# Performance work log

Hardware: AMD Instinct MI355X
Metric: run time of the kernel (lower is better)

Reference implementation:

```python
import jax, jax.numpy as jnp
import numpy as np

B, S, IN, E, H, FF, L = 8, 1024, 128, 512, 8, 2048, 4
HD = E // H
EPS = 1e-5


def make_pe(seq_len, d_model):
    position = np.arange(seq_len, dtype=np.float32)[:, None]
    div_term = np.exp(np.arange(0, d_model, 2, dtype=np.float32) * (-np.log(10000.0) / d_model))
    pe = np.zeros((seq_len, d_model), dtype=np.float32)
    pe[:, 0::2] = np.sin(position * div_term)
    pe[:, 1::2] = np.cos(position * div_term)
    return jnp.asarray(pe)


def setup_inputs() -> dict:
    key = jax.random.key(0)
    ks = jax.random.split(key, 16)
    s = 0.02
    return {
        "src": jax.random.normal(ks[0], (B, S, IN), jnp.float32),
        "distances": jax.random.uniform(ks[1], (B, S, S), jnp.float32),
        "proj_w": jax.random.normal(ks[2], (E, IN), jnp.float32) * s,
        "proj_b": jnp.zeros((E,), jnp.float32),
        "bn_g": jnp.ones((E,), jnp.float32),
        "bn_b": jnp.zeros((E,), jnp.float32),
        "in_proj_w": jax.random.normal(ks[3], (3 * E, E), jnp.float32) * s,
        "in_proj_b": jnp.zeros((3 * E,), jnp.float32),
        "dist_scale": jnp.array(1.0, jnp.float32),
        "lin1_w": jax.random.normal(ks[4], (FF, E), jnp.float32) * s,
        "lin1_b": jnp.zeros((FF,), jnp.float32),
        "lin2_w": jax.random.normal(ks[5], (E, FF), jnp.float32) * s,
        "lin2_b": jnp.zeros((E,), jnp.float32),
        "n1_g": jnp.ones((E,), jnp.float32),
        "n1_b": jnp.zeros((E,), jnp.float32),
        "n2_g": jnp.ones((E,), jnp.float32),
        "n2_b": jnp.zeros((E,), jnp.float32),
    }


def layernorm(x, g, b):
    m = jnp.mean(x, axis=-1, keepdims=True)
    v = jnp.var(x, axis=-1, keepdims=True)
    return (x - m) * jax.lax.rsqrt(v + EPS) * g + b


def reference(src, distances, proj_w, proj_b, bn_g, bn_b, in_proj_w, in_proj_b,
              dist_scale, lin1_w, lin1_b, lin2_w, lin2_b, n1_g, n1_b, n2_g, n2_b):
    # input projection
    x = jnp.einsum('bsi,ei->bse', src, proj_w) + proj_b  # [B,S,E]
    # BatchNorm1d over flattened (B*S) dim, training-mode batch stats
    xf = x.reshape(-1, E)
    mu = jnp.mean(xf, axis=0)
    var = jnp.var(xf, axis=0)
    x = ((xf - mu) * jax.lax.rsqrt(var + EPS) * bn_g + bn_b).reshape(B, S, E)
    # positional encoding
    x = x + make_pe(S, E)[None]
    # distance bias (same for every layer)
    dmax = jnp.max(distances, axis=-1, keepdims=True)
    dist_bias = jnp.exp(dist_scale * (1.0 - distances / dmax))  # [B,S,S]
    scale = 1.0 / jnp.sqrt(jnp.float32(HD))
    # num_layers iterations of the SAME (shared-parameter) layer
    for _ in range(L):
        qkv = jnp.einsum('bse,fe->bsf', x, in_proj_w) + in_proj_b  # [B,S,3E]
        q, k, v = jnp.split(qkv, 3, axis=-1)
        q = q.reshape(B, S, H, HD).transpose(0, 2, 1, 3)
        k = k.reshape(B, S, H, HD).transpose(0, 2, 1, 3)
        scores = jnp.einsum('bhqd,bhkd->bhqk', q, k) * scale  # [B,H,S,S]
        attn = jax.nn.softmax(scores, axis=-1)
        avg_w = jnp.mean(attn, axis=1)  # head-averaged weights [B,S,S]
        w = avg_w * dist_bias
        w = w / jnp.sum(w, axis=-1, keepdims=True)
        # NOTE: original bmm uses raw layer input as value (no V/out projection)
        attn_out = jnp.einsum('bqk,bke->bqe', w, x)
        x = layernorm(x + attn_out, n1_g, n1_b)
        ff = jnp.einsum('bsf,ef->bse', jax.nn.relu(jnp.einsum('bse,fe->bsf', x, lin1_w) + lin1_b), lin2_w) + lin2_b
        x = layernorm(x + ff, n2_g, n2_b)
    return x
```

## Files before the change

### kernel.cpp

```cpp
#include <hip/hip_runtime.h>
#include <hip/hip_bf16.h>
#include <math.h>

#define Bz 8
#define Sz 1024
#define INz 128
#define Ez 512
#define Hz 8
#define HDz 64
#define FFz 2048
#define Lz 4
#define Nz (Bz*Sz)
#define EPSf 1e-5f

typedef __attribute__((ext_vector_type(8))) short short8;
typedef __attribute__((ext_vector_type(4))) float floatx4;
#define MFMA16(a,b,c) __builtin_amdgcn_mfma_f32_16x16x32_bf16(a,b,c,0,0,0)

typedef __hip_bfloat16 bf16;

__device__ inline float b2f(bf16 v) { return __bfloat162float(v); }
__device__ inline bf16 f2b(float v) { return __float2bfloat16(v); }

__device__ inline void gload16(const bf16* g, bf16* lds_base)
{
  __builtin_amdgcn_global_load_lds(
      (const __attribute__((address_space(1))) void*)g,
      (__attribute__((address_space(3))) void*)lds_base,
      16, 0, 0);
}

#define FENCE() asm volatile("" ::: "memory")
#define PB() do { FENCE(); __builtin_amdgcn_s_barrier(); FENCE(); } while (0)
#define VMCNT0() asm volatile("s_waitcnt vmcnt(0)" ::: "memory")
#define VMCNT8() asm volatile("s_waitcnt vmcnt(8)" ::: "memory")

__global__ __launch_bounds__(256) void cast_f2b(const float* __restrict__ in,
    bf16* __restrict__ out, int n)
{
  int i = blockIdx.x * 256 + threadIdx.x;
  if (i < n) out[i] = f2b(in[i]);
}

__global__ __launch_bounds__(512, 1) void gemm256(
    const bf16* __restrict__ A, const bf16* __restrict__ Wm,
    const float* __restrict__ bias, bf16* __restrict__ Cb,
    int N, int K, int relu)
{
  int gx = gridDim.x, nwg = gx * gridDim.y;
  int flat = blockIdx.y * gx + blockIdx.x;
  if (!(nwg & 7)) {
    int cpx = nwg >> 3;
    flat = (flat & 7) * cpx + (flat >> 3);
  }
  int bm = (flat / gx) * 256, bn = (flat % gx) * 256;
  __shared__ __align__(16) bf16 As0[256][64], Bs0[256][64];
  __shared__ __align__(16) bf16 As1[256][64], Bs1[256][64];
  int t = threadIdx.x, wave = t >> 6, lane = t & 63;
  int wm = (wave >> 2) * 128, wn = (wave & 3) * 64;
  int fr = lane & 15, fo = lane >> 4;
  int w8 = wave * 8, lrow = lane >> 3;
  int sc8 = ((lane & 7) ^ (lrow & 7)) * 8;
  floatx4 acc[8][4];
  #pragma unroll
  for (int i = 0; i < 8; ++i)
    #pragma unroll
    for (int j = 0; j < 4; ++j) acc[i][j] = (floatx4){0.f, 0.f, 0.f, 0.f};

  #define STAGE8(DA, DB, kk) do {                                           \
    _Pragma("unroll")                                                        \
    for (int c_ = 0; c_ < 4; ++c_) {                                         \
      int row_ = c_ * 64 + w8 + lrow;                                        \
      gload16(A  + (size_t)(bm + row_) * K + (kk) + sc8, &DA[c_ * 64 + w8][0]);\
      gload16(Wm + (size_t)(bn + row_) * K + (kk) + sc8, &DB[c_ * 64 + w8][0]);\
    } } while (0)

  #define TILE(AA, BB, SA, SB, kk, DOSTAGE) do {                            \
    _Pragma("unroll")                                                        \
    for (int q_ = 0; q_ < 4; ++q_) {                                         \
      short8 a_[4][2], bf_[2][2];                                            \
      _Pragma("unroll")                                                      \
      for (int j_ = 0; j_ < 4; ++j_) {                                       \
        int row_ = wm + ((q_ >> 1) * 4 + j_) * 16 + fr;                      \
        a_[j_][0] = *(const short8*)&AA[row_][((fo) ^ (fr & 7)) * 8];        \
        a_[j_][1] = *(const short8*)&AA[row_][((4 + fo) ^ (fr & 7)) * 8];    \
      }                                                                      \
      _Pragma("unroll")                                                      \
      for (int g_ = 0; g_ < 2; ++g_) {                                       \
        int row_ = wn + ((q_ & 1) * 2 + g_) * 16 + fr;                       \
        bf_[g_][0] = *(const short8*)&BB[row_][((fo) ^ (fr & 7)) * 8];       \
        bf_[g_][1] = *(const short8*)&BB[row_][((4 + fo) ^ (fr & 7)) * 8];   \
      }                                                                      \
      if ((DOSTAGE) && q_ == 0) STAGE8(SA, SB, kk);                          \
      PB();                                                                  \
      __builtin_amdgcn_s_setprio(1);                                         \
      _Pragma("unroll")                                                      \
      for (int j_ = 0; j_ < 4; ++j_)                                         \
        _Pragma("unroll")                                                    \
        for (int g_ = 0; g_ < 2; ++g_) {                                     \
          int fi_ = (q_ >> 1) * 4 + j_, gi_ = (q_ & 1) * 2 + g_;             \
          acc[fi_][gi_] = MFMA16(a_[j_][0], bf_[g_][0], acc[fi_][gi_]);      \
          acc[fi_][gi_] = MFMA16(a_[j_][1], bf_[g_][1], acc[fi_][gi_]);      \
        }                                                                    \
      __builtin_amdgcn_s_setprio(0);                                         \
      if (q_ == 3) VMCNT0();                                                 \
      PB();                                                                  \
    } } while (0)

  int nt = K >> 6;
  STAGE8(As0, Bs0, 0);
  STAGE8(As1, Bs1, 64);
  VMCNT8();
  PB();
  TILE(As0, Bs0, As0, Bs0, 0, 0);
  for (int i = 1; i + 2 < nt; i += 2) {
    TILE(As1, Bs1, As0, Bs0, (i + 1) * 64, 1);
    TILE(As0, Bs0, As1, Bs1, (i + 2) * 64, 1);
  }
  TILE(As1, Bs1, As0, Bs0, 0, 0);
  #undef STAGE8
  #undef TILE

  #pragma unroll
  for (int f = 0; f < 8; ++f) {
    #pragma unroll
    for (int r = 0; r < 4; ++r) {
      int row = bm + wm + f * 16 + (lane >> 4) * 4 + r;
      #pragma unroll
      for (int g = 0; g < 4; ++g) {
        int col = bn + wn + g * 16 + fr;
        float v = acc[f][g][r] + (bias ? bias[col] : 0.f);
        if (relu) v = fmaxf(v, 0.f);
        Cb[(size_t)row * N + col] = f2b(v);
      }
    }
  }
}

__global__ __launch_bounds__(256) void gemm_bt(
    const bf16* __restrict__ A, const bf16* __restrict__ Wm,
    const float* __restrict__ bias, float* __restrict__ Cf,
    bf16* __restrict__ Cb, const float* __restrict__ rowscale,
    int M, int N, int K, long sA, long sW, long sC, int relu)
{
  int z = blockIdx.z;
  A  += (size_t)z * sA;
  Wm += (size_t)z * sW;
  if (rowscale) rowscale += (size_t)z * M;
  size_t cbase = (size_t)z * sC;
  int bm = blockIdx.y * 128, bn = blockIdx.x * 128;
  __shared__ __align__(16) bf16 As0[128][64], Bs0[128][64];
  __shared__ __align__(16) bf16 As1[128][64], Bs1[128][64];
  int t = threadIdx.x, wave = t >> 6, lane = t & 63;
  int wm = (wave >> 1) * 64, wn = (wave & 1) * 64;
  int fr = lane & 15, fo = lane >> 4;
  int srow = lane >> 3;
  int scol = ((lane & 7) ^ srow) * 8;
  floatx4 acc[4][4];
  #pragma unroll
  for (int i = 0; i < 4; ++i)
    #pragma unroll
    for (int j = 0; j < 4; ++j) acc[i][j] = (floatx4){0.f, 0.f, 0.f, 0.f};

  #define STAGE(Ad, Bd, kk) do {                                            \
    _Pragma("unroll")                                                        \
    for (int i_ = 0; i_ < 4; ++i_) {                                         \
      int chunk_ = wave * 4 + i_;                                            \
      int row_ = chunk_ * 8 + srow;                                          \
      gload16(A  + (size_t)(bm + row_) * K + (kk) + scol, &Ad[chunk_ * 8][0]);\
      gload16(Wm + (size_t)(bn + row_) * K + (kk) + scol, &Bd[chunk_ * 8][0]);\
    } } while (0)

  #define COMPUTE(Ad, Bd) do {                                               \
    _Pragma("unroll")                                                        \
    for (int ks_ = 0; ks_ < 2; ++ks_) {                                      \
      int sw_ = ((ks_ * 4 + fo) ^ (fr & 7)) * 8;                             \
      short8 af_[4], bf_[4];                                                 \
      _Pragma("unroll")                                                      \
      for (int rt_ = 0; rt_ < 4; ++rt_)                                      \
        af_[rt_] = *(const short8*)&Ad[wm + rt_ * 16 + fr][sw_];             \
      _Pragma("unroll")                                                      \
      for (int ct_ = 0; ct_ < 4; ++ct_)                                      \
        bf_[ct_] = *(const short8*)&Bd[wn + ct_ * 16 + fr][sw_];             \
      _Pragma("unroll")                                                      \
      for (int rt_ = 0; rt_ < 4; ++rt_)                                      \
        _Pragma("unroll")                                                    \
        for (int ct_ = 0; ct_ < 4; ++ct_)                                    \
          acc[rt_][ct_] = MFMA16(af_[rt_], bf_[ct_], acc[rt_][ct_]);         \
    } } while (0)

  STAGE(As0, Bs0, 0);
  __syncthreads();
  for (int k0 = 0; k0 < K; k0 += 128) {
    if (k0 + 64 < K) STAGE(As1, Bs1, k0 + 64);
    COMPUTE(As0, Bs0);
    __syncthreads();
    if (k0 + 64 < K) {
      if (k0 + 128 < K) STAGE(As0, Bs0, k0 + 128);
      COMPUTE(As1, Bs1);
      __syncthreads();
    }
  }
  #undef STAGE
  #undef COMPUTE

  #pragma unroll
  for (int rt = 0; rt < 4; ++rt) {
    #pragma unroll
    for (int r = 0; r < 4; ++r) {
      int row = bm + wm + rt * 16 + (lane >> 4) * 4 + r;
      float rs = rowscale ? (1.f / rowscale[row]) : 1.f;
      #pragma unroll
      for (int ct = 0; ct < 4; ++ct) {
        int col = bn + wn + ct * 16 + fr;
        float v = acc[rt][ct][r] + (bias ? bias[col] : 0.f);
        if (relu) v = fmaxf(v, 0.f);
        v *= rs;
        if (Cf) Cf[cbase + (size_t)row * N + col] = v;
        if (Cb) Cb[cbase + (size_t)row * N + col] = f2b(v);
      }
    }
  }
}

__global__ __launch_bounds__(256) void bn_stats(const float* __restrict__ x, float* __restrict__ st)
{
  int c = blockIdx.x;
  float s = 0.f, q = 0.f;
  for (int r = threadIdx.x; r < Nz; r += 256) {
    float v = x[(size_t)r * Ez + c];
    s += v; q += v * v;
  }
  for (int o = 32; o; o >>= 1) { s += __shfl_down(s, o); q += __shfl_down(q, o); }
  __shared__ float shs[4], shq[4];
  int w = threadIdx.x >> 6;
  if ((threadIdx.x & 63) == 0) { shs[w] = s; shq[w] = q; }
  __syncthreads();
  if (threadIdx.x == 0) {
    s = shs[0] + shs[1] + shs[2] + shs[3];
    q = shq[0] + shq[1] + shq[2] + shq[3];
    float mu = s / (float)Nz;
    float var = q / (float)Nz - mu * mu;
    st[c] = mu;
    st[Ez + c] = rsqrtf(var + EPSf);
  }
}

__global__ __launch_bounds__(256) void bn_apply_pe(const float* __restrict__ x0,
    const float* __restrict__ st, const float* __restrict__ g,
    const float* __restrict__ b, float* __restrict__ x, bf16* __restrict__ xb)
{
  int idx = blockIdx.x * 256 + threadIdx.x;
  int c = idx & (Ez - 1);
  int r = idx >> 9;
  int s = r & (Sz - 1);
  float dt = expf((float)(c & ~1) * (-9.210340371976184f / (float)Ez));
  float ang = (float)s * dt;
  float pe = (c & 1) ? cosf(ang) : sinf(ang);
  float mu = st[c], rs = st[Ez + c];
  float v = (x0[idx] - mu) * rs * g[c] + b[c] + pe;
  x[idx] = v;
  xb[idx] = f2b(v);
}

__global__ __launch_bounds__(256) void dist_bias_k(const float* __restrict__ dist,
    const float* __restrict__ dsc, bf16* __restrict__ db)
{
  size_t base = (size_t)blockIdx.x * Sz;
  float m = -1e30f;
  for (int j = threadIdx.x; j < Sz; j += 256) m = fmaxf(m, dist[base + j]);
  for (int o = 32; o; o >>= 1) m = fmaxf(m, __shfl_down(m, o));
  __shared__ float sh[4];
  if ((threadIdx.x & 63) == 0) sh[threadIdx.x >> 6] = m;
  __syncthreads();
  m = fmaxf(fmaxf(sh[0], sh[1]), fmaxf(sh[2], sh[3]));
  float sc = dsc[0];
  float inv = 1.f / m;
  for (int j = threadIdx.x; j < Sz; j += 256)
    db[base + j] = f2b(expf(sc * (1.f - dist[base + j] * inv)));
}

__global__ __launch_bounds__(256) void transpose_xb(const bf16* __restrict__ xb,
    bf16* __restrict__ xT)
{
  int b = blockIdx.z, e0 = blockIdx.y * 32, s0 = blockIdx.x * 32;
  __shared__ bf16 T[32][40];
  int t = threadIdx.x, row = t >> 3, c = t & 7;
  *(ushort4*)&T[row][c * 4] = *(const ushort4*)(xb + (size_t)(b * Sz + s0 + row) * Ez + e0 + c * 4);
  __syncthreads();
  ushort4 v;
  unsigned short* vp = (unsigned short*)&v;
  #pragma unroll
  for (int i = 0; i < 4; ++i) vp[i] = *(const unsigned short*)&T[c * 4 + i][row];
  *(ushort4*)(xT + ((size_t)b * Ez + e0 + row) * Sz + s0 + c * 4) = v;
}

__global__ __launch_bounds__(256) void attn_stats2(const bf16* __restrict__ qk,
    float* __restrict__ stats, float* __restrict__ den)
{
  int qt = blockIdx.x, h = blockIdx.y, b = blockIdx.z;
  int q0 = qt * 64;
  int t = threadIdx.x, wave = t >> 6, lane = t & 63;
  if (h == 0 && t < 64) den[(size_t)b * Sz + q0 + t] = 0.f;
  __shared__ bf16 Qs[64][72];
  __shared__ bf16 Ks[128][72];
  int fr = lane & 15, fo = (lane >> 4) * 8;
  #pragma unroll
  for (int i = 0; i < 2; ++i) {
    int idx = i * 256 + t, row = idx >> 3, c4 = idx & 7;
    *(float4*)&Qs[row][c4 * 8] =
      *(const float4*)(qk + (size_t)(b * Sz + q0 + row) * 1024 + h * 64 + c4 * 8);
  }
  __syncthreads();
  short8 aq0 = *(const short8*)&Qs[wave * 16 + fr][fo];
  short8 aq1 = *(const short8*)&Qs[wave * 16 + fr][32 + fo];
  float m_run[4] = {-1e30f, -1e30f, -1e30f, -1e30f};
  float z_run[4] = {0.f, 0.f, 0.f, 0.f};
  for (int k0 = 0; k0 < Sz; k0 += 128) {
    __syncthreads();
    #pragma unroll
    for (int i = 0; i < 4; ++i) {
      int idx = i * 256 + t, row = idx >> 3, c4 = idx & 7;
      *(float4*)&Ks[row][c4 * 8] =
        *(const float4*)(qk + (size_t)(b * Sz + k0 + row) * 1024 + 512 + h * 64 + c4 * 8);
    }
    __syncthreads();
    float sc[8][4];
    #pragma unroll
    for (int j = 0; j < 8; ++j) {
      floatx4 a4 = (floatx4){0.f, 0.f, 0.f, 0.f};
      short8 b0 = *(const short8*)&Ks[j * 16 + fr][fo];
      short8 b1 = *(const short8*)&Ks[j * 16 + fr][32 + fo];
      a4 = MFMA16(aq0, b0, a4);
      a4 = MFMA16(aq1, b1, a4);
      #pragma unroll
      for (int r = 0; r < 4; ++r) sc[j][r] = a4[r] * 0.125f;
    }
    #pragma unroll
    for (int r = 0; r < 4; ++r) {
      float vm = sc[0][r];
      #pragma unroll
      for (int j = 1; j < 8; ++j) vm = fmaxf(vm, sc[j][r]);
      #pragma unroll
      for (int o = 1; o < 16; o <<= 1) vm = fmaxf(vm, __shfl_xor(vm, o, 16));
      float mn = fmaxf(m_run[r], vm);
      float zb = 0.f;
      #pragma unroll
      for (int j = 0; j < 8; ++j) zb += __expf(sc[j][r] - mn);
      #pragma unroll
      for (int o = 1; o < 16; o <<= 1) zb += __shfl_xor(zb, o, 16);
      z_run[r] = z_run[r] * __expf(m_run[r] - mn) + zb;
      m_run[r] = mn;
    }
  }
  if (fr == 0) {
    int qb = q0 + wave * 16 + (lane >> 4) * 4;
    #pragma unroll
    for (int r = 0; r < 4; ++r) {
      size_t o = ((size_t)(b * Hz + h) * Sz + qb + r) * 2;
      stats[o] = m_run[r];
      stats[o + 1] = z_run[r];
    }
  }
}

__global__ __launch_bounds__(256) void scores_bias(const bf16* __restrict__ qk,
    const bf16* __restrict__ db, const float* __restrict__ stats,
    bf16* __restrict__ aw, float* __restrict__ den)
{
  int kt = blockIdx.x, qt = blockIdx.y, b = blockIdx.z;
  int q0 = qt * 128, k0 = kt * 128;
  __shared__ bf16 Qs[128][72];
  __shared__ bf16 Ks[128][72];
  __shared__ float mS[128][9];
  __shared__ float ziS[128][9];
  int t = threadIdx.x, wave = t >> 6, lane = t & 63;
  int fr = lane & 15, fo = (lane >> 4) * 8;
  int wm = (wave >> 1) * 64, wn = (wave & 1) * 64;

  #pragma unroll
  for (int i = 0; i < 4; ++i) {
    int lin = i * 256 + t, h = lin >> 7, q = lin & 127;
    const float* sp = stats + ((size_t)(b * Hz + h) * Sz + q0 + q) * 2;
    mS[q][h] = sp[0];
    ziS[q][h] = 1.f / sp[1];
  }

  floatx4 pac[4][4];
  #pragma unroll
  for (int i = 0; i < 4; ++i)
    #pragma unroll
    for (int j = 0; j < 4; ++j) pac[i][j] = (floatx4){0.f, 0.f, 0.f, 0.f};

  for (int h = 0; h < 8; ++h) {
    __syncthreads();
    #pragma unroll
    for (int i = 0; i < 4; ++i) {
      int idx = i * 256 + t, row = idx >> 3, c4 = idx & 7;
      *(float4*)&Qs[row][c4 * 8] =
        *(const float4*)(qk + (size_t)(b * Sz + q0 + row) * 1024 + h * 64 + c4 * 8);
      *(float4*)&Ks[row][c4 * 8] =
        *(const float4*)(qk + (size_t)(b * Sz + k0 + row) * 1024 + 512 + h * 64 + c4 * 8);
    }
    __syncthreads();
    short8 bfv0[4], bfv1[4];
    #pragma unroll
    for (int ct = 0; ct < 4; ++ct) {
      bfv0[ct] = *(const short8*)&Ks[wn + ct * 16 + fr][fo];
      bfv1[ct] = *(const short8*)&Ks[wn + ct * 16 + fr][32 + fo];
    }
    #pragma unroll
    for (int rt = 0; rt < 4; ++rt) {
      short8 af0 = *(const short8*)&Qs[wm + rt * 16 + fr][fo];
      short8 af1 = *(const short8*)&Qs[wm + rt * 16 + fr][32 + fo];
      floatx4 sc[4];
      #pragma unroll
      for (int ct = 0; ct < 4; ++ct) {
        floatx4 z4 = (floatx4){0.f, 0.f, 0.f, 0.f};
        z4 = MFMA16(af0, bfv0[ct], z4);
        sc[ct] = MFMA16(af1, bfv1[ct], z4);
      }
      #pragma unroll
      for (int r = 0; r < 4; ++r) {
        int qloc = wm + rt * 16 + (lane >> 4) * 4 + r;
        float m = mS[qloc][h], zi = ziS[qloc][h];
        #pragma unroll
        for (int ct = 0; ct < 4; ++ct)
          pac[rt][ct][r] += __expf(sc[ct][r] * 0.125f - m) * zi;
      }
    }
  }

  #pragma unroll
  for (int rt = 0; rt < 4; ++rt) {
    #pragma unroll
    for (int r = 0; r < 4; ++r) {
      int qloc = wm + rt * 16 + (lane >> 4) * 4 + r;
      size_t rowoff = (size_t)(b * Sz + q0 + qloc) * Sz + k0;
      float rsum = 0.f;
      #pragma unroll
      for (int ct = 0; ct < 4; ++ct) {
        int kloc = wn + ct * 16 + fr;
        float p = pac[rt][ct][r] * 0.125f * b2f(db[rowoff + kloc]);
        aw[rowoff + kloc] = f2b(p);
        rsum += p;
      }
      #pragma unroll
      for (int o = 1; o < 16; o <<= 1) rsum += __shfl_xor(rsum, o, 16);
      if (fr == 0) atomicAdd(den + (size_t)b * Sz + q0 + qloc, rsum);
    }
  }
}

__global__ __launch_bounds__(256) void add_ln(const float* __restrict__ xin,
    const float* __restrict__ dly, const float* __restrict__ g,
    const float* __restrict__ bb, float* __restrict__ xout, bf16* __restrict__ xbout)
{
  size_t base = (size_t)blockIdx.x * Ez;
  int t = threadIdx.x;
  float2 xi = *(const float2*)(xin + base + t * 2);
  float2 dl = *(const float2*)(dly + base + t * 2);
  float a0 = xi.x + dl.x;
  float a1 = xi.y + dl.y;
  float s = a0 + a1, q = a0 * a0 + a1 * a1;
  for (int o = 32; o; o >>= 1) { s += __shfl_down(s, o); q += __shfl_down(q, o); }
  __shared__ float shs[4], shq[4];
  if ((t & 63) == 0) { shs[t >> 6] = s; shq[t >> 6] = q; }
  __syncthreads();
  s = shs[0] + shs[1] + shs[2] + shs[3];
  q = shq[0] + shq[1] + shq[2] + shq[3];
  float mu = s * (1.f / Ez);
  float var = q * (1.f / Ez) - mu * mu;
  float rs = rsqrtf(var + EPSf);
  float v0 = (a0 - mu) * rs * g[t * 2] + bb[t * 2];
  float v1 = (a1 - mu) * rs * g[t * 2 + 1] + bb[t * 2 + 1];
  float2 vo; vo.x = v0; vo.y = v1;
  *(float2*)(xout + base + t * 2) = vo;
  bf16 b0 = f2b(v0), b1 = f2b(v1);
  ushort2 pk;
  pk.x = *(unsigned short*)&b0;
  pk.y = *(unsigned short*)&b1;
  *(ushort2*)(xbout + base + t * 2) = pk;
}

extern "C" void kernel_launch(void* const* d_in, const int* in_sizes, int n_in,
                              void* d_out, int out_size, void* d_ws, size_t ws_size,
                              hipStream_t stream)
{
  const float* src        = (const float*)d_in[0];
  const float* distances  = (const float*)d_in[1];
  const float* proj_w     = (const float*)d_in[2];
  const float* proj_b     = (const float*)d_in[3];
  const float* bn_g       = (const float*)d_in[4];
  const float* bn_b       = (const float*)d_in[5];
  const float* in_proj_w  = (const float*)d_in[6];
  const float* in_proj_b  = (const float*)d_in[7];
  const float* dist_scale = (const float*)d_in[8];
  const float* lin1_w     = (const float*)d_in[9];
  const float* lin1_b     = (const float*)d_in[10];
  const float* lin2_w     = (const float*)d_in[11];
  const float* lin2_b     = (const float*)d_in[12];
  const float* n1_g       = (const float*)d_in[13];
  const float* n1_b       = (const float*)d_in[14];
  const float* n2_g       = (const float*)d_in[15];
  const float* n2_b       = (const float*)d_in[16];

  float* x = (float*)d_out;

  float* stats = (float*)d_ws;
  float* den   = stats + 131072;
  float* bnst  = den + 8192;
  float* aout  = bnst + 1024;
  float* x0    = aout;
  bf16* db_b = (bf16*)(aout + (size_t)Nz * Ez);
  bf16* Rqk  = db_b + (size_t)Bz * Sz * Sz;
  bf16* qk   = Rqk;
  bf16* aw   = Rqk + (size_t)Nz * 1024;
  bf16* ff1  = Rqk;
  bf16* xb   = Rqk + (size_t)Nz * FFz;
  bf16* xT   = xb + (size_t)Nz * Ez;
  bf16* srcb = xT + (size_t)Bz * Ez * Sz;
  bf16* wpr  = srcb + (size_t)Nz * INz;
  bf16* wqk  = wpr + Ez * INz;
  bf16* wl1  = wqk + 1024 * Ez;
  bf16* wl2  = wl1 + FFz * Ez;

  cast_f2b<<<(Nz * INz) / 256, 256, 0, stream>>>(src, srcb, Nz * INz);
  cast_f2b<<<(Ez * INz + 255) / 256, 256, 0, stream>>>(proj_w, wpr, Ez * INz);
  cast_f2b<<<(1024 * Ez) / 256, 256, 0, stream>>>(in_proj_w, wqk, 1024 * Ez);
  cast_f2b<<<(FFz * Ez) / 256, 256, 0, stream>>>(lin1_w, wl1, FFz * Ez);
  cast_f2b<<<(Ez * FFz) / 256, 256, 0, stream>>>(lin2_w, wl2, Ez * FFz);

  gemm_bt<<<dim3(Ez / 128, Nz / 128, 1), 256, 0, stream>>>(
      srcb, wpr, proj_b, x0, nullptr, nullptr, Nz, Ez, INz, 0, 0, 0, 0);
  bn_stats<<<Ez, 256, 0, stream>>>(x0, bnst);
  bn_apply_pe<<<(Nz * Ez) / 256, 256, 0, stream>>>(x0, bnst, bn_g, bn_b, x, xb);
  dist_bias_k<<<Bz * Sz, 256, 0, stream>>>(distances, dist_scale, db_b);

  for (int l = 0; l < Lz; ++l) {
    transpose_xb<<<dim3(Sz / 32, Ez / 32, Bz), 256, 0, stream>>>(xb, xT);
    gemm_bt<<<dim3(1024 / 128, Nz / 128, 1), 256, 0, stream>>>(
        xb, wqk, in_proj_b, nullptr, qk, nullptr, Nz, 1024, Ez, 0, 0, 0, 0);
    attn_stats2<<<dim3(Sz / 64, Hz, Bz), 256, 0, stream>>>(qk, stats, den);
    scores_bias<<<dim3(Sz / 128, Sz / 128, Bz), 256, 0, stream>>>(qk, db_b, stats, aw, den);
    gemm_bt<<<dim3(Ez / 128, Sz / 128, Bz), 256, 0, stream>>>(
        aw, xT, nullptr, aout, nullptr, den,
        Sz, Ez, Sz, (long)Sz * Sz, (long)Ez * Sz, (long)Sz * Ez, 0);
    add_ln<<<Nz, 256, 0, stream>>>(x, aout, n1_g, n1_b, x, xb);
    gemm256<<<dim3(FFz / 256, Nz / 256), 512, 0, stream>>>(
        xb, wl1, lin1_b, ff1, FFz, Ez, 1);
    gemm_bt<<<dim3(Ez / 128, Nz / 128, 1), 256, 0, stream>>>(
        ff1, wl2, lin2_b, aout, nullptr, nullptr, Nz, Ez, FFz, 0, 0, 0, 0);
    add_ln<<<Nz, 256, 0, stream>>>(x, aout, n2_g, n2_b, x, xb);
  }
}
```

Measured before the change: 1.138 ms.

## Double-buffer Q/K tiles with async direct-to-LDS loads and XOR swizzle

Rewrites the attention stats and score-bias kernels to stage Q/K tiles with gload16 (global-to-LDS loads) into two LDS buffers. The load of the next tile overlaps the MFMA and softmax work on the current one. The padded [72] LDS rows become unpadded [64] rows with an XOR swizzle to avoid bank conflicts. In exchange it doubles LDS use per block, which may lower occupancy, and it relies on the swizzle matching between the stores and the fragment reads.

```diff
diff --git a/kernel.cpp b/kernel.cpp
--- a/kernel.cpp
+++ b/kernel.cpp
@@ -302,57 +302,73 @@
   int q0 = qt * 64;
   int t = threadIdx.x, wave = t >> 6, lane = t & 63;
   if (h == 0 && t < 64) den[(size_t)b * Sz + q0 + t] = 0.f;
-  __shared__ bf16 Qs[64][72];
-  __shared__ bf16 Ks[128][72];
-  int fr = lane & 15, fo = (lane >> 4) * 8;
+  __shared__ __align__(16) bf16 Qs[64][64];
+  __shared__ __align__(16) bf16 Ks0[128][64], Ks1[128][64];
+  int fr = lane & 15, fo = lane >> 4;
+  int srow = lane >> 3;
+  int scol = ((lane & 7) ^ srow) * 8;
+  int sw0 = ((fo) ^ (fr & 7)) * 8, sw1 = ((4 + fo) ^ (fr & 7)) * 8;
+
   #pragma unroll
   for (int i = 0; i < 2; ++i) {
-    int idx = i * 256 + t, row = idx >> 3, c4 = idx & 7;
-    *(float4*)&Qs[row][c4 * 8] =
-      *(const float4*)(qk + (size_t)(b * Sz + q0 + row) * 1024 + h * 64 + c4 * 8);
-  }
-  __syncthreads();
-  short8 aq0 = *(const short8*)&Qs[wave * 16 + fr][fo];
-  short8 aq1 = *(const short8*)&Qs[wave * 16 + fr][32 + fo];
+    int chunk = wave * 2 + i, row = chunk * 8 + srow;
+    gload16(qk + (size_t)(b * Sz + q0 + row) * 1024 + h * 64 + scol, &Qs[chunk * 8][0]);
+  }
+  #define STAGEK(Kd, kk) do {                                                \
+    _Pragma("unroll")                                                        \
+    for (int i_ = 0; i_ < 4; ++i_) {                                         \
+      int chunk_ = wave * 4 + i_, row_ = chunk_ * 8 + srow;                  \
+      gload16(qk + (size_t)(b * Sz + (kk) + row_) * 1024 + 512 + h * 64 + scol,\
+              &Kd[chunk_ * 8][0]);                                           \
+    } } while (0)
+
+  STAGEK(Ks0, 0);
+  __syncthreads();
+  short8 aq0 = *(const short8*)&Qs[wave * 16 + fr][sw0];
+  short8 aq1 = *(const short8*)&Qs[wave * 16 + fr][sw1];
   float m_run[4] = {-1e30f, -1e30f, -1e30f, -1e30f};
   float z_run[4] = {0.f, 0.f, 0.f, 0.f};
-  for (int k0 = 0; k0 < Sz; k0 += 128) {
+
+  #define KCOMP(Kd) do {                                                     \
+    float sc[8][4];                                                          \
+    _Pragma("unroll")                                                        \
+    for (int j = 0; j < 8; ++j) {                                            \
+      floatx4 a4 = (floatx4){0.f, 0.f, 0.f, 0.f};                            \
+      short8 b0 = *(const short8*)&Kd[j * 16 + fr][sw0];                     \
+      short8 b1 = *(const short8*)&Kd[j * 16 + fr][sw1];                     \
+      a4 = MFMA16(aq0, b0, a4);                                              \
+      a4 = MFMA16(aq1, b1, a4);                                              \
+      _Pragma("unroll")                                                      \
+      for (int r = 0; r < 4; ++r) sc[j][r] = a4[r] * 0.125f;                 \
+    }                                                                        \
+    _Pragma("unroll")                                                        \
+    for (int r = 0; r < 4; ++r) {                                            \
+      float vm = sc[0][r];                                                   \
+      _Pragma("unroll")                                                      \
+      for (int j = 1; j < 8; ++j) vm = fmaxf(vm, sc[j][r]);                  \
+      _Pragma("unroll")                                                      \
+      for (int o = 1; o < 16; o <<= 1) vm = fmaxf(vm, __shfl_xor(vm, o, 16));\
+      float mn = fmaxf(m_run[r], vm);                                        \
+      float zb = 0.f;                                                        \
+      _Pragma("unroll")                                                      \
+      for (int j = 0; j < 8; ++j) zb += __expf(sc[j][r] - mn);               \
+      _Pragma("unroll")                                                      \
+      for (int o = 1; o < 16; o <<= 1) zb += __shfl_xor(zb, o, 16);          \
+      z_run[r] = z_run[r] * __expf(m_run[r] - mn) + zb;                      \
+      m_run[r] = mn;                                                         \
+    } } while (0)
+
+  for (int k0 = 0; k0 < Sz; k0 += 256) {
+    STAGEK(Ks1, k0 + 128);
+    KCOMP(Ks0);
     __syncthreads();
-    #pragma unroll
-    for (int i = 0; i < 4; ++i) {
-      int idx = i * 256 + t, row = idx >> 3, c4 = idx & 7;
-      *(float4*)&Ks[row][c4 * 8] =
-        *(const float4*)(qk + (size_t)(b * Sz + k0 + row) * 1024 + 512 + h * 64 + c4 * 8);
-    }
+    if (k0 + 256 < Sz) STAGEK(Ks0, k0 + 256);
+    KCOMP(Ks1);
     __syncthreads();
-    float sc[8][4];
-    #pragma unroll
-    for (int j = 0; j < 8; ++j) {
-      floatx4 a4 = (floatx4){0.f, 0.f, 0.f, 0.f};
-      short8 b0 = *(const short8*)&Ks[j * 16 + fr][fo];
-      short8 b1 = *(const short8*)&Ks[j * 16 + fr][32 + fo];
-      a4 = MFMA16(aq0, b0, a4);
-      a4 = MFMA16(aq1, b1, a4);
-      #pragma unroll
-      for (int r = 0; r < 4; ++r) sc[j][r] = a4[r] * 0.125f;
-    }
-    #pragma unroll
-    for (int r = 0; r < 4; ++r) {
-      float vm = sc[0][r];
-      #pragma unroll
-      for (int j = 1; j < 8; ++j) vm = fmaxf(vm, sc[j][r]);
-      #pragma unroll
-      for (int o = 1; o < 16; o <<= 1) vm = fmaxf(vm, __shfl_xor(vm, o, 16));
-      float mn = fmaxf(m_run[r], vm);
-      float zb = 0.f;
-      #pragma unroll
-      for (int j = 0; j < 8; ++j) zb += __expf(sc[j][r] - mn);
-      #pragma unroll
-      for (int o = 1; o < 16; o <<= 1) zb += __shfl_xor(zb, o, 16);
-      z_run[r] = z_run[r] * __expf(m_run[r] - mn) + zb;
-      m_run[r] = mn;
-    }
-  }
+  }
+  #undef STAGEK
+  #undef KCOMP
+
   if (fr == 0) {
     int qb = q0 + wave * 16 + (lane >> 4) * 4;
     #pragma unroll
@@ -370,13 +386,16 @@
 {
   int kt = blockIdx.x, qt = blockIdx.y, b = blockIdx.z;
   int q0 = qt * 128, k0 = kt * 128;
-  __shared__ bf16 Qs[128][72];
-  __shared__ bf16 Ks[128][72];
+  __shared__ __align__(16) bf16 Qs0[128][64], Ks0[128][64];
+  __shared__ __align__(16) bf16 Qs1[128][64], Ks1[128][64];
   __shared__ float mS[128][9];
   __shared__ float ziS[128][9];
   int t = threadIdx.x, wave = t >> 6, lane = t & 63;
-  int fr = lane & 15, fo = (lane >> 4) * 8;
+  int fr = lane & 15, fo = lane >> 4;
   int wm = (wave >> 1) * 64, wn = (wave & 1) * 64;
+  int srow = lane >> 3;
+  int scol = ((lane & 7) ^ srow) * 8;
+  int sw0 = ((fo) ^ (fr & 7)) * 8, sw1 = ((4 + fo) ^ (fr & 7)) * 8;
 
   #pragma unroll
   for (int i = 0; i < 4; ++i) {
@@ -392,44 +411,57 @@
     #pragma unroll
     for (int j = 0; j < 4; ++j) pac[i][j] = (floatx4){0.f, 0.f, 0.f, 0.f};
 
-  for (int h = 0; h < 8; ++h) {
+  #define STAGEH(Qd, Kd, hh) do {                                            \
+    _Pragma("unroll")                                                        \
+    for (int i_ = 0; i_ < 4; ++i_) {                                         \
+      int chunk_ = wave * 4 + i_, row_ = chunk_ * 8 + srow;                  \
+      gload16(qk + (size_t)(b * Sz + q0 + row_) * 1024 + (hh) * 64 + scol,   \
+              &Qd[chunk_ * 8][0]);                                           \
+      gload16(qk + (size_t)(b * Sz + k0 + row_) * 1024 + 512 + (hh) * 64 + scol,\
+              &Kd[chunk_ * 8][0]);                                           \
+    } } while (0)
+
+  #define HCOMP(Qd, Kd, hh) do {                                             \
+    short8 bfv0[4], bfv1[4];                                                 \
+    _Pragma("unroll")                                                        \
+    for (int ct = 0; ct < 4; ++ct) {                                         \
+      bfv0[ct] = *(const short8*)&Kd[wn + ct * 16 + fr][sw0];                \
+      bfv1[ct] = *(const short8*)&Kd[wn + ct * 16 + fr][sw1];                \
+    }                                                                        \
+    _Pragma("unroll")                                                        \
+    for (int rt = 0; rt < 4; ++rt) {                                         \
+      short8 af0 = *(const short8*)&Qd[wm + rt * 16 + fr][sw0];              \
+      short8 af1 = *(const short8*)&Qd[wm + rt * 16 + fr][sw1];              \
+      floatx4 sc[4];                                                         \
+      _Pragma("unroll")                                                      \
+      for (int ct = 0; ct < 4; ++ct) {                                       \
+        floatx4 z4 = (floatx4){0.f, 0.f, 0.f, 0.f};                          \
+        z4 = MFMA16(af0, bfv0[ct], z4);                                      \
+        sc[ct] = MFMA16(af1, bfv1[ct], z4);                                  \
+      }                                                                      \
+      _Pragma("unroll")                                                      \
+      for (int r = 0; r < 4; ++r) {                                          \
+        int qloc = wm + rt * 16 + (lane >> 4) * 4 + r;                       \
+        float m = mS[qloc][hh], zi = ziS[qloc][hh];                          \
+        _Pragma("unroll")                                                    \
+        for (int ct = 0; ct < 4; ++ct)                                       \
+          pac[rt][ct][r] += __expf(sc[ct][r] * 0.125f - m) * zi;             \
+      }                                                                      \
+    } } while (0)
+
+  STAGEH(Qs0, Ks0, 0);
+  __syncthreads();
+  #pragma unroll
+  for (int h = 0; h < 8; h += 2) {
+    STAGEH(Qs1, Ks1, h + 1);
+    HCOMP(Qs0, Ks0, h);
     __syncthreads();
-    #pragma unroll
-    for (int i = 0; i < 4; ++i) {
-      int idx = i * 256 + t, row = idx >> 3, c4 = idx & 7;
-      *(float4*)&Qs[row][c4 * 8] =
-        *(const float4*)(qk + (size_t)(b * Sz + q0 + row) * 1024 + h * 64 + c4 * 8);
-      *(float4*)&Ks[row][c4 * 8] =
-        *(const float4*)(qk + (size_t)(b * Sz + k0 + row) * 1024 + 512 + h * 64 + c4 * 8);
-    }
+    if (h + 2 < 8) STAGEH(Qs0, Ks0, h + 2);
+    HCOMP(Qs1, Ks1, h + 1);
     __syncthreads();
-    short8 bfv0[4], bfv1[4];
-    #pragma unroll
-    for (int ct = 0; ct < 4; ++ct) {
-      bfv0[ct] = *(const short8*)&Ks[wn + ct * 16 + fr][fo];
-      bfv1[ct] = *(const short8*)&Ks[wn + ct * 16 + fr][32 + fo];
-    }
-    #pragma unroll
-    for (int rt = 0; rt < 4; ++rt) {
-      short8 af0 = *(const short8*)&Qs[wm + rt * 16 + fr][fo];
-      short8 af1 = *(const short8*)&Qs[wm + rt * 16 + fr][32 + fo];
-      floatx4 sc[4];
-      #pragma unroll
-      for (int ct = 0; ct < 4; ++ct) {
-        floatx4 z4 = (floatx4){0.f, 0.f, 0.f, 0.f};
-        z4 = MFMA16(af0, bfv0[ct], z4);
-        sc[ct] = MFMA16(af1, bfv1[ct], z4);
-      }
-      #pragma unroll
-      for (int r = 0; r < 4; ++r) {
-        int qloc = wm + rt * 16 + (lane >> 4) * 4 + r;
-        float m = mS[qloc][h], zi = ziS[qloc][h];
-        #pragma unroll
-        for (int ct = 0; ct < 4; ++ct)
-          pac[rt][ct][r] += __expf(sc[ct][r] * 0.125f - m) * zi;
-      }
-    }
-  }
+  }
+  #undef STAGEH
+  #undef HCOMP
 
   #pragma unroll
   for (int rt = 0; rt < 4; ++rt) {
```

Measured after the change: 1.563 ms. +37.3%, slower.

## Double-buffer Q/K head tiles in scores_bias with async loads and XOR swizzle

Applied to the files above, without the earlier changes.

The scores_bias kernel now keeps two LDS buffers for the per-head Q and K tiles and fills them with direct global-to-LDS loads (gload16). The next head is staged while the current head is computed, which halves the barriers per head and hides global load latency. Padded rows are replaced by an XOR-swizzled 64-column layout to avoid LDS bank conflicts. This doubles LDS use for the tiles, which may reduce occupancy.

```diff
diff --git a/kernel.cpp b/kernel.cpp
--- a/kernel.cpp
+++ b/kernel.cpp
@@ -370,13 +370,16 @@
 {
   int kt = blockIdx.x, qt = blockIdx.y, b = blockIdx.z;
   int q0 = qt * 128, k0 = kt * 128;
-  __shared__ bf16 Qs[128][72];
-  __shared__ bf16 Ks[128][72];
+  __shared__ __align__(16) bf16 Qs0[128][64], Ks0[128][64];
+  __shared__ __align__(16) bf16 Qs1[128][64], Ks1[128][64];
   __shared__ float mS[128][9];
   __shared__ float ziS[128][9];
   int t = threadIdx.x, wave = t >> 6, lane = t & 63;
-  int fr = lane & 15, fo = (lane >> 4) * 8;
+  int fr = lane & 15, fo = lane >> 4;
   int wm = (wave >> 1) * 64, wn = (wave & 1) * 64;
+  int srow = lane >> 3;
+  int scol = ((lane & 7) ^ srow) * 8;
+  int sw0 = ((fo) ^ (fr & 7)) * 8, sw1 = ((4 + fo) ^ (fr & 7)) * 8;
 
   #pragma unroll
   for (int i = 0; i < 4; ++i) {
@@ -392,44 +395,57 @@
     #pragma unroll
     for (int j = 0; j < 4; ++j) pac[i][j] = (floatx4){0.f, 0.f, 0.f, 0.f};
 
-  for (int h = 0; h < 8; ++h) {
+  #define STAGEH(Qd, Kd, hh) do {                                            \
+    _Pragma("unroll")                                                        \
+    for (int i_ = 0; i_ < 4; ++i_) {                                         \
+      int chunk_ = wave * 4 + i_, row_ = chunk_ * 8 + srow;                  \
+      gload16(qk + (size_t)(b * Sz + q0 + row_) * 1024 + (hh) * 64 + scol,   \
+              &Qd[chunk_ * 8][0]);                                           \
+      gload16(qk + (size_t)(b * Sz + k0 + row_) * 1024 + 512 + (hh) * 64 + scol,\
+              &Kd[chunk_ * 8][0]);                                           \
+    } } while (0)
+
+  #define HCOMP(Qd, Kd, hh) do {                                             \
+    short8 bfv0[4], bfv1[4];                                                 \
+    _Pragma("unroll")                                                        \
+    for (int ct = 0; ct < 4; ++ct) {                                         \
+      bfv0[ct] = *(const short8*)&Kd[wn + ct * 16 + fr][sw0];                \
+      bfv1[ct] = *(const short8*)&Kd[wn + ct * 16 + fr][sw1];                \
+    }                                                                        \
+    _Pragma("unroll")                                                        \
+    for (int rt = 0; rt < 4; ++rt) {                                         \
+      short8 af0 = *(const short8*)&Qd[wm + rt * 16 + fr][sw0];              \
+      short8 af1 = *(const short8*)&Qd[wm + rt * 16 + fr][sw1];              \
+      floatx4 sc[4];                                                         \
+      _Pragma("unroll")                                                      \
+      for (int ct = 0; ct < 4; ++ct) {                                       \
+        floatx4 z4 = (floatx4){0.f, 0.f, 0.f, 0.f};                          \
+        z4 = MFMA16(af0, bfv0[ct], z4);                                      \
+        sc[ct] = MFMA16(af1, bfv1[ct], z4);                                  \
+      }                                                                      \
+      _Pragma("unroll")                                                      \
+      for (int r = 0; r < 4; ++r) {                                          \
+        int qloc = wm + rt * 16 + (lane >> 4) * 4 + r;                       \
+        float m = mS[qloc][hh], zi = ziS[qloc][hh];                          \
+        _Pragma("unroll")                                                    \
+        for (int ct = 0; ct < 4; ++ct)                                       \
+          pac[rt][ct][r] += __expf(sc[ct][r] * 0.125f - m) * zi;             \
+      }                                                                      \
+    } } while (0)
+
+  STAGEH(Qs0, Ks0, 0);
+  __syncthreads();
+  #pragma unroll 1
+  for (int h = 0; h < 8; h += 2) {
+    STAGEH(Qs1, Ks1, h + 1);
+    HCOMP(Qs0, Ks0, h);
     __syncthreads();
-    #pragma unroll
-    for (int i = 0; i < 4; ++i) {
-      int idx = i * 256 + t, row = idx >> 3, c4 = idx & 7;
-      *(float4*)&Qs[row][c4 * 8] =
-        *(const float4*)(qk + (size_t)(b * Sz + q0 + row) * 1024 + h * 64 + c4 * 8);
-      *(float4*)&Ks[row][c4 * 8] =
-        *(const float4*)(qk + (size_t)(b * Sz + k0 + row) * 1024 + 512 + h * 64 + c4 * 8);
-    }
+    if (h + 2 < 8) STAGEH(Qs0, Ks0, h + 2);
+    HCOMP(Qs1, Ks1, h + 1);
     __syncthreads();
-    short8 bfv0[4], bfv1[4];
-    #pragma unroll
-    for (int ct = 0; ct < 4; ++ct) {
-      bfv0[ct] = *(const short8*)&Ks[wn + ct * 16 + fr][fo];
-      bfv1[ct] = *(const short8*)&Ks[wn + ct * 16 + fr][32 + fo];
-    }
-    #pragma unroll
-    for (int rt = 0; rt < 4; ++rt) {
-      short8 af0 = *(const short8*)&Qs[wm + rt * 16 + fr][fo];
-      short8 af1 = *(const short8*)&Qs[wm + rt * 16 + fr][32 + fo];
-      floatx4 sc[4];
-      #pragma unroll
-      for (int ct = 0; ct < 4; ++ct) {
-        floatx4 z4 = (floatx4){0.f, 0.f, 0.f, 0.f};
-        z4 = MFMA16(af0, bfv0[ct], z4);
-        sc[ct] = MFMA16(af1, bfv1[ct], z4);
-      }
-      #pragma unroll
-      for (int r = 0; r < 4; ++r) {
-        int qloc = wm + rt * 16 + (lane >> 4) * 4 + r;
-        float m = mS[qloc][h], zi = ziS[qloc][h];
-        #pragma unroll
-        for (int ct = 0; ct < 4; ++ct)
-          pac[rt][ct][r] += __expf(sc[ct][r] * 0.125f - m) * zi;
-      }
-    }
-  }
+  }
+  #undef STAGEH
+  #undef HCOMP
 
   #pragma unroll
   for (int rt = 0; rt < 4; ++rt) {
```

After: 1.127 ms (median of 2 runs). No clear change (-0.9%).
